# Performance work log

Hardware: AMD Instinct MI355X
Metric: run time of the kernel (lower is better)

## Reference

```python
import jax, jax.numpy as jnp
import numpy as np

EPS = 1e-5
K = 20


def knn(x, k):
    # x: (b, c, n) -> idx (b, n, k) of nearest neighbors (negative sq. distance, top-k)
    xx = jnp.sum(x * x, axis=1)                      # (b, n)
    inner = jnp.einsum('bcn,bcm->bnm', x, x)         # (b, n, n)
    neg_dist = -xx[:, :, None] + 2.0 * inner - xx[:, None, :]
    _, idx = jax.lax.top_k(neg_dist, k)
    return idx


def graph_feature(x, k):
    # x: (b, c, n) -> (b, 2c, n, k) with [neighbor - center, center]
    b, c, n = x.shape
    idx = knn(x, k)                                   # (b, n, k)
    xt = jnp.transpose(x, (0, 2, 1))                  # (b, n, c)
    nbr = jax.vmap(lambda xb, ib: xb[ib])(xt, idx)    # (b, n, k, c)
    ctr = xt[:, :, None, :]                           # (b, n, 1, c)
    f = jnp.concatenate([nbr - ctr, jnp.broadcast_to(ctr, (b, n, k, c))], axis=-1)
    return jnp.transpose(f, (0, 3, 1, 2))             # (b, 2c, n, k)


def conv_bn_lrelu2d(f, W, gamma, beta):
    # 1x1 Conv2d (no bias) + BatchNorm2d (batch stats) + LeakyReLU(0.2)
    y = jnp.einsum('oc,bcnk->bonk', W, f)
    m = jnp.mean(y, axis=(0, 2, 3), keepdims=True)
    v = jnp.var(y, axis=(0, 2, 3), keepdims=True)
    y = (y - m) * jax.lax.rsqrt(v + EPS) * gamma[None, :, None, None] + beta[None, :, None, None]
    return jnp.where(y >= 0, y, 0.2 * y)


def conv_bn_lrelu1d(f, W, gamma, beta):
    y = jnp.einsum('oc,bcn->bon', W, f)
    m = jnp.mean(y, axis=(0, 2), keepdims=True)
    v = jnp.var(y, axis=(0, 2), keepdims=True)
    y = (y - m) * jax.lax.rsqrt(v + EPS) * gamma[None, :, None] + beta[None, :, None]
    return jnp.where(y >= 0, y, 0.2 * y)


def setup_inputs() -> dict:
    key = jax.random.key(0)
    ks = jax.random.split(key, 16)
    B, N = 8, 1024
    x = jax.random.normal(ks[0], (B, 3, N), dtype=jnp.float32)
    def w(k_, o, c):
        return jax.random.normal(k_, (o, c), dtype=jnp.float32) * (1.0 / np.sqrt(c))
    W1 = w(ks[1], 64, 6)
    W2 = w(ks[2], 64, 128)
    W3 = w(ks[3], 128, 128)
    W4 = w(ks[4], 256, 256)
    W5 = w(ks[5], 1024, 512)
    def gb(k_, c):
        k1, k2 = jax.random.split(k_)
        return (1.0 + 0.1 * jax.random.normal(k1, (c,), dtype=jnp.float32),
                0.1 * jax.random.normal(k2, (c,), dtype=jnp.float32))
    g1, b1 = gb(ks[6], 64)
    g2, b2 = gb(ks[7], 64)
    g3, b3 = gb(ks[8], 128)
    g4, b4 = gb(ks[9], 256)
    g5, b5 = gb(ks[10], 1024)
    return dict(x=x, W1=W1, g1=g1, b1=b1, W2=W2, g2=g2, b2=b2,
                W3=W3, g3=g3, b3=b3, W4=W4, g4=g4, b4=b4,
                W5=W5, g5=g5, b5=b5)


def reference(x, W1, g1, b1, W2, g2, b2, W3, g3, b3, W4, g4, b4, W5, g5, b5):
    f = graph_feature(x, K)                           # (b, 6, n, k)
    x1 = jnp.max(conv_bn_lrelu2d(f, W1, g1, b1), axis=-1)   # (b, 64, n)
    f = graph_feature(x1, K)
    x2 = jnp.max(conv_bn_lrelu2d(f, W2, g2, b2), axis=-1)   # (b, 64, n)
    f = graph_feature(x2, K)
    x3 = jnp.max(conv_bn_lrelu2d(f, W3, g3, b3), axis=-1)   # (b, 128, n)
    f = graph_feature(x3, K)
    x4 = jnp.max(conv_bn_lrelu2d(f, W4, g4, b4), axis=-1)   # (b, 256, n)
    cat = jnp.concatenate([x1, x2, x3, x4], axis=1)          # (b, 512, n)
    y = conv_bn_lrelu1d(cat, W5, g5, b5)                     # (b, 1024, n)
    return jnp.max(y, axis=-1)                               # (b, 1024) global feature
```

## Files before the change

### kernel.cpp

```cpp
#include <hip/hip_runtime.h>
#include <math.h>

#define KK 20
#define NPTS 1024
#define BB 8
#define EPSF 1e-5f

__device__ __forceinline__ void select20f(float (&d)[16], int lane, int* orow)
{
  int keep = 0;
  for (int s = 0; s < KK; ++s) {
    float bd = d[0]; int bj = 0;
    #pragma unroll
    for (int j = 1; j < 16; ++j)
      if (d[j] > bd) { bd = d[j]; bj = j; }
    int bi = bj * 64 + lane;
    #pragma unroll
    for (int o = 1; o < 64; o <<= 1) {
      float od = __shfl_xor(bd, o, 64);
      int   oi = __shfl_xor(bi, o, 64);
      if (od > bd || (od == bd && oi < bi)) { bd = od; bi = oi; }
    }
    if (lane == s) keep = bi;
    if ((bi & 63) == lane) {
      int jw = bi >> 6;
      #pragma unroll
      for (int j = 0; j < 16; ++j)
        if (j == jw) d[j] = -INFINITY;
    }
  }
  if (lane < KK) orow[lane] = keep;
}

template <int C, int CEFF>
__global__ __launch_bounds__(512, 8) void knn8_kernel(
    const float* __restrict__ x, long bstride,
    int* __restrict__ idx_out)
{
  const int t = threadIdx.x, w = t >> 6, lane = t & 63;
  const int b = blockIdx.y;
  const int n0 = blockIdx.x * 8;
  const int p = n0 + w;
  __shared__ float xs2[2][NPTS * 2];
  __shared__ float xxs[NPTS];
  const float* xb = x + (long)b * bstride;

  float2 r2[4];
  #pragma unroll
  for (int j = 0; j < 4; ++j) {
    if (j < CEFF) r2[j] = *(const float2*)&xb[(long)j * NPTS + 2 * t];
    else          r2[j] = make_float2(0.f, 0.f);
  }

  float xx0 = 0.f, xx1 = 0.f;
  float dot[16];
  #pragma unroll
  for (int j = 0; j < 16; ++j) dot[j] = 0.f;

  for (int c0 = 0; c0 < C; c0 += 4) {
    __syncthreads();
    {
      float4 w0 = make_float4(r2[0].x, r2[1].x, r2[0].y, r2[1].y);
      float4 w1 = make_float4(r2[2].x, r2[3].x, r2[2].y, r2[3].y);
      *(float4*)&xs2[0][4 * t] = w0;
      *(float4*)&xs2[1][4 * t] = w1;
    }
    #pragma unroll
    for (int j = 0; j < 4; ++j) {
      xx0 = fmaf(r2[j].x, r2[j].x, xx0);
      xx1 = fmaf(r2[j].y, r2[j].y, xx1);
    }
    __syncthreads();
    if (c0 + 4 < C) {
      #pragma unroll
      for (int j = 0; j < 4; ++j)
        r2[j] = *(const float2*)&xb[(long)(c0 + 4 + j) * NPTS + 2 * t];
    }
    #pragma unroll
    for (int pr = 0; pr < 2; ++pr) {
      float2 cab = *(const float2*)&xs2[pr][p * 2];
      #pragma unroll
      for (int j = 0; j < 16; ++j) {
        float2 v = *(const float2*)&xs2[pr][(j * 64 + lane) * 2];
        dot[j] = fmaf(cab.x, v.x, dot[j]);
        dot[j] = fmaf(cab.y, v.y, dot[j]);
      }
    }
  }
  *(float2*)&xxs[2 * t] = make_float2(xx0, xx1);
  __syncthreads();

  const float xxP = xxs[p];
  #pragma unroll
  for (int j = 0; j < 16; ++j) {
    float xm = xxs[j * 64 + lane];
    dot[j] = (2.0f * dot[j] - xxP) - xm;
  }
  select20f(dot, lane, idx_out + ((long)b * NPTS + p) * KK);
}

template <typename AccT, int C, int O, int CB2, int TN>
__global__ __launch_bounds__(256) void cg_kernel(
    const float* __restrict__ x, long bstride,
    const float* __restrict__ W,
    AccT* __restrict__ Yc,
    AccT* __restrict__ G, long gbs)
{
  const int t = threadIdx.x, b = blockIdx.y;
  const int o = t & (O - 1);
  const int nbase = (t / O) * 16;
  const int nn0 = blockIdx.x * TN;
  __shared__ float s_wd[CB2 * O];
  __shared__ float s_w1[CB2 * O];
  __shared__ float s_xs[CB2 * TN];
  const float* xb = x + (long)b * bstride;

  AccT accC[16], accG[16];
  #pragma unroll
  for (int j = 0; j < 16; ++j) { accC[j] = (AccT)0; accG[j] = (AccT)0; }

  for (int c0 = 0; c0 < C; c0 += CB2) {
    __syncthreads();
    for (int i = t; i < CB2 * O; i += 256) {
      int oo = i / CB2, cc = i - oo * CB2;
      float a  = W[(long)oo * (2 * C) + c0 + cc];
      float b2 = W[(long)oo * (2 * C) + C + c0 + cc];
      s_wd[cc * O + oo] = b2 - a;
      s_w1[cc * O + oo] = a;
    }
    for (int i = t; i < CB2 * TN; i += 256) {
      int cc = i / TN, nn = i - cc * TN;
      s_xs[cc * TN + nn] = xb[(long)(c0 + cc) * NPTS + nn0 + nn];
    }
    __syncthreads();
    #pragma unroll
    for (int cc = 0; cc < CB2; ++cc) {
      float wd  = s_wd[cc * O + o];
      float w1v = s_w1[cc * O + o];
      #pragma unroll
      for (int j = 0; j < 16; ++j) {
        AccT xv = (AccT)s_xs[cc * TN + nbase + j];
        accC[j] += (AccT)wd  * xv;
        accG[j] += (AccT)w1v * xv;
      }
    }
  }
  #pragma unroll
  for (int j = 0; j < 16; ++j) {
    int n = nn0 + nbase + j;
    Yc[((long)b * NPTS + n) * O + o] = accC[j];
    G[(long)b * gbs + (long)n * O + o] = accG[j];
  }
}

template <typename AccT, int O, int NPT, int ITERS>
__global__ __launch_bounds__(256) void ec_max_kernel(
    const int* __restrict__ idx,
    const AccT* __restrict__ G, long gbs,
    const AccT* __restrict__ Yc,
    double* __restrict__ sums,
    AccT* __restrict__ yraw)
{
  const int t = threadIdx.x, b = blockIdx.y;
  const int o = t & (O - 1);
  const int np = t / O;
  const int LP = NPT * ITERS;
  const int n0 = blockIdx.x * LP;

  __shared__ int s_jj[8 * KK];
  __shared__ double reds[256];
  __shared__ double redq[256];

  for (int i = t; i < LP * KK; i += 256) {
    int l = i / KK, kk = i - l * KK;
    s_jj[i] = idx[((long)b * NPTS + n0 + l) * KK + kk];
  }
  __syncthreads();

  const AccT* Gb = G + (long)b * gbs + o;
  double accS = 0.0, accQ = 0.0;
  #pragma unroll
  for (int it = 0; it < ITERS; ++it) {
    const int l = it * NPT + np;
    const int n = n0 + l;
    AccT y0 = Yc[((long)b * NPTS + n) * O + o];
    AccT ps = (AccT)0, pq = (AccT)0, pm = (AccT)(-INFINITY);
    #pragma unroll
    for (int k = 0; k < KK; ++k) {
      int j = s_jj[l * KK + k];
      AccT v = Gb[(long)j * O] + y0;
      ps += v; pq += v * v;
      pm = (v > pm) ? v : pm;
    }
    yraw[((long)b * NPTS + n) * O + o] = pm;
    accS += (double)ps; accQ += (double)pq;
  }
  __syncthreads();
  reds[t] = accS; redq[t] = accQ;
  __syncthreads();
  if (t < O) {
    double s = 0.0, q = 0.0;
    #pragma unroll
    for (int g = 0; g < NPT; ++g) { s += reds[g * O + t]; q += redq[g * O + t]; }
    atomicAdd(&sums[t], s);
    atomicAdd(&sums[1024 + t], q);
  }
}

template <typename AccT, int O, int OL>
__global__ __launch_bounds__(256) void ec_norm(
    const AccT* __restrict__ yraw, const double* __restrict__ sums,
    const float* __restrict__ gamma, const float* __restrict__ beta,
    float* __restrict__ xout)
{
  int i = blockIdx.x * 256 + threadIdx.x;
  int n = i & (NPTS - 1);
  int o = (i >> 10) & (O - 1);
  int b = i >> (10 + OL);
  const double cnt = (double)BB * NPTS * KK;
  double m = sums[o] / cnt;
  double var = sums[1024 + o] / cnt - m * m;
  double inv = 1.0 / sqrt(var + (double)EPSF);
  AccT y = yraw[((long)b * NPTS + n) * O + o];
  AccT v = (y - (AccT)m) * (AccT)inv * (AccT)gamma[o] + (AccT)beta[o];
  v = (v >= (AccT)0) ? v : (AccT)0.2 * v;
  xout[(long)b * (512L * NPTS) + (long)o * NPTS + n] = (float)v;
}

__device__ inline unsigned fkey(float f) {
  unsigned u = __float_as_uint(f);
  return (u & 0x80000000u) ? ~u : (u | 0x80000000u);
}
__device__ inline float keyf(unsigned k) {
  return __uint_as_float((k & 0x80000000u) ? (k ^ 0x80000000u) : ~k);
}

#define WST2 260

__global__ __launch_bounds__(256, 4) void fin_fused(
    const float* __restrict__ cat, const float* __restrict__ W5,
    double* __restrict__ sums, unsigned* __restrict__ mkeys)
{
  const int nt = blockIdx.x, ot = blockIdx.y, t = threadIdx.x;
  const int w = t >> 6, lane = t & 63;
  const int col0 = nt * 32;
  const int b = col0 >> 10;
  const int nb = col0 & 1023;

  __shared__ float sm[16 * WST2 + 16 * 32];
  float* s_w = sm;
  float* s_f = sm + 16 * WST2;

  const int wrow0 = t >> 2, wcq = (t & 3) * 4;
  const float* wbase = W5 + ((long)(ot * 256 + wrow0)) * 512 + wcq;
  const int fcc = (2 * t) >> 5, fnn = (2 * t) & 31;
  const float* fbase = cat + ((long)b * 512 + fcc) * 1024 + nb + fnn;

  float4 rw[4];
  float2 rf;
  #pragma unroll
  for (int q = 0; q < 4; ++q)
    rw[q] = *(const float4*)&wbase[(long)(64 * q) * 512];
  rf = *(const float2*)fbase;

  float acc[4][8];
  #pragma unroll
  for (int r = 0; r < 4; ++r)
    #pragma unroll
    for (int j = 0; j < 8; ++j) acc[r][j] = 0.f;

  for (int c0 = 0; c0 < 512; c0 += 16) {
    __syncthreads();
    #pragma unroll
    for (int q = 0; q < 4; ++q) {
      float e[4] = {rw[q].x, rw[q].y, rw[q].z, rw[q].w};
      #pragma unroll
      for (int j = 0; j < 4; ++j)
        s_w[(wcq + j) * WST2 + wrow0 + 64 * q] = e[j];
    }
    *(float2*)&s_f[fcc * 32 + fnn] = rf;
    __syncthreads();
    if (c0 + 16 < 512) {
      #pragma unroll
      for (int q = 0; q < 4; ++q)
        rw[q] = *(const float4*)&wbase[(long)(64 * q) * 512 + c0 + 16];
      rf = *(const float2*)&fbase[(long)(c0 + 16) * 1024];
    }
    #pragma unroll
    for (int cc = 0; cc < 16; ++cc) {
      float4 wA = *(const float4*)&s_w[cc * WST2 + lane * 4];
      float4 f0 = *(const float4*)&s_f[cc * 32 + w * 8];
      float4 f1 = *(const float4*)&s_f[cc * 32 + w * 8 + 4];
      float wa[4] = {wA.x, wA.y, wA.z, wA.w};
      float fv[8] = {f0.x, f0.y, f0.z, f0.w, f1.x, f1.y, f1.z, f1.w};
      #pragma unroll
      for (int r = 0; r < 4; ++r)
        #pragma unroll
        for (int j = 0; j < 8; ++j)
          acc[r][j] += wa[r] * fv[j];
    }
  }

  float psum[4], psq[4], pmx[4];
  #pragma unroll
  for (int r = 0; r < 4; ++r) {
    psum[r] = 0.f; psq[r] = 0.f; pmx[r] = -INFINITY;
    #pragma unroll
    for (int j = 0; j < 8; ++j) {
      float v = acc[r][j];
      psum[r] += v; psq[r] += v * v; pmx[r] = fmaxf(pmx[r], v);
    }
  }
  __syncthreads();
  float* red_s = sm;
  float* red_q = sm + 1024;
  float* red_m = sm + 2048;
  #pragma unroll
  for (int r = 0; r < 4; ++r) {
    int oo = lane * 4 + r;
    red_s[w * 256 + oo] = psum[r];
    red_q[w * 256 + oo] = psq[r];
    red_m[w * 256 + oo] = pmx[r];
  }
  __syncthreads();
  {
    int oo = t;
    float s = 0.f, q = 0.f, m = -INFINITY;
    #pragma unroll
    for (int ww = 0; ww < 4; ++ww) {
      s += red_s[ww * 256 + oo];
      q += red_q[ww * 256 + oo];
      m = fmaxf(m, red_m[ww * 256 + oo]);
    }
    int o = ot * 256 + oo;
    atomicAdd(&sums[o], (double)s);
    atomicAdd(&sums[1024 + o], (double)q);
    atomicMax(&mkeys[b * 1024 + o], fkey(m));
  }
}

__global__ __launch_bounds__(256) void fin_norm(
    const unsigned* __restrict__ mkeys, const double* __restrict__ sums,
    const float* __restrict__ g, const float* __restrict__ bt,
    float* __restrict__ out)
{
  int i = blockIdx.x * 256 + threadIdx.x;
  int o = i & 1023;
  double m = sums[o] / 8192.0;
  double var = sums[1024 + o] / 8192.0 - m * m;
  float inv = (float)(1.0 / sqrt(var + (double)EPSF));
  float y = keyf(mkeys[i]);
  float v = (y - (float)m) * inv * g[o] + bt[o];
  out[i] = (v >= 0.f) ? v : 0.2f * v;
}

extern "C" void kernel_launch(void* const* d_in, const int* in_sizes, int n_in,
                              void* d_out, int out_size, void* d_ws, size_t ws_size,
                              hipStream_t stream)
{
  (void)in_sizes; (void)n_in; (void)out_size; (void)ws_size;
  const float* x0 = (const float*)d_in[0];
  const float* W1 = (const float*)d_in[1];
  const float* g1 = (const float*)d_in[2];
  const float* b1 = (const float*)d_in[3];
  const float* W2 = (const float*)d_in[4];
  const float* g2 = (const float*)d_in[5];
  const float* b2 = (const float*)d_in[6];
  const float* W3 = (const float*)d_in[7];
  const float* g3 = (const float*)d_in[8];
  const float* b3 = (const float*)d_in[9];
  const float* W4 = (const float*)d_in[10];
  const float* g4 = (const float*)d_in[11];
  const float* b4 = (const float*)d_in[12];
  const float* W5 = (const float*)d_in[13];
  const float* g5 = (const float*)d_in[14];
  const float* b5 = (const float*)d_in[15];
  float* outp = (float*)d_out;

  char* w = (char*)d_ws;
  double*   sums   = (double*)w;   w += 5 * 2048 * sizeof(double);
  unsigned* mkeys  = (unsigned*)w; w += (size_t)BB * 1024 * sizeof(unsigned);
  int*      idxbuf = (int*)w;      w += (size_t)BB * NPTS * KK * sizeof(int);
  char*     yraw   = w;            w += (size_t)BB * NPTS * 128 * sizeof(double);
  char*     ycbuf  = w;            w += (size_t)BB * NPTS * 128 * sizeof(double);
  float*    cat    = (float*)w;

  double* sumsL[5] = {sums, sums + 2048, sums + 4096, sums + 6144, sums + 8192};

  const long catbs = 512L * NPTS;
  float* gbase = cat + 256 * NPTS;

  dim3 gknn(NPTS / 8, BB);

  hipMemsetAsync(sums, 0, 5 * 2048 * sizeof(double) + (size_t)BB * 1024 * sizeof(unsigned),
                 stream);

  knn8_kernel<4, 3><<<gknn, 512, 0, stream>>>(x0, 3L * NPTS, idxbuf);
  cg_kernel<double, 3, 64, 3, 64><<<dim3(NPTS / 64, BB), 256, 0, stream>>>(
      x0, 3L * NPTS, W1, (double*)ycbuf, (double*)gbase, catbs / 2);
  ec_max_kernel<double, 64, 4, 2><<<dim3(NPTS / 8, BB), 256, 0, stream>>>(
      idxbuf, (const double*)gbase, catbs / 2, (const double*)ycbuf,
      sumsL[0], (double*)yraw);
  ec_norm<double, 64, 6><<<BB * 64 * NPTS / 256, 256, 0, stream>>>(
      (const double*)yraw, sumsL[0], g1, b1, cat);

  knn8_kernel<64, 64><<<gknn, 512, 0, stream>>>(cat, catbs, idxbuf);
  cg_kernel<double, 64, 64, 16, 64><<<dim3(NPTS / 64, BB), 256, 0, stream>>>(
      cat, catbs, W2, (double*)ycbuf, (double*)gbase, catbs / 2);
  ec_max_kernel<double, 64, 4, 2><<<dim3(NPTS / 8, BB), 256, 0, stream>>>(
      idxbuf, (const double*)gbase, catbs / 2, (const double*)ycbuf,
      sumsL[1], (double*)yraw);
  ec_norm<double, 64, 6><<<BB * 64 * NPTS / 256, 256, 0, stream>>>(
      (const double*)yraw, sumsL[1], g2, b2, cat + 64 * NPTS);

  knn8_kernel<64, 64><<<gknn, 512, 0, stream>>>(cat + 64 * NPTS, catbs, idxbuf);
  cg_kernel<double, 64, 128, 16, 32><<<dim3(NPTS / 32, BB), 256, 0, stream>>>(
      cat + 64 * NPTS, catbs, W3, (double*)ycbuf, (double*)gbase, catbs / 2);
  ec_max_kernel<double, 128, 2, 4><<<dim3(NPTS / 8, BB), 256, 0, stream>>>(
      idxbuf, (const double*)gbase, catbs / 2, (const double*)ycbuf,
      sumsL[2], (double*)yraw);
  ec_norm<double, 128, 7><<<BB * 128 * NPTS / 256, 256, 0, stream>>>(
      (const double*)yraw, sumsL[2], g3, b3, cat + 128 * NPTS);

  knn8_kernel<128, 128><<<gknn, 512, 0, stream>>>(cat + 128 * NPTS, catbs, idxbuf);
  cg_kernel<float, 128, 256, 16, 16><<<dim3(NPTS / 16, BB), 256, 0, stream>>>(
      cat + 128 * NPTS, catbs, W4, (float*)ycbuf, gbase, catbs);
  ec_max_kernel<float, 256, 1, 4><<<dim3(NPTS / 4, BB), 256, 0, stream>>>(
      idxbuf, (const float*)gbase, catbs, (const float*)ycbuf,
      sumsL[3], (float*)yraw);
  ec_norm<float, 256, 8><<<BB * 256 * NPTS / 256, 256, 0, stream>>>(
      (const float*)yraw, sumsL[3], g4, b4, cat + 256 * NPTS);

  dim3 gf(256, 4);
  fin_fused<<<gf, 256, 0, stream>>>(cat, W5, sumsL[4], mkeys);
  fin_norm<<<BB * 1024 / 256, 256, 0, stream>>>(mkeys, sumsL[4], g5, b5, outp);
}
```

Measured before the change: 779.5 us.

## Compute two query points per wave in kNN and use DPP reductions

The kNN kernel now has each wave handle two query points, so every shared-memory candidate load is reused for two dot products, and the grid is halved to match. The top-20 selection replaces the linear 16-way argmax with a tree reduction and does the first four cross-lane steps with DPP moves instead of shuffles. The cost is more registers per thread (launch bounds lowered to 4 blocks) and two selection passes done one after another per wave, which reduces occupancy and latency hiding.

New measurement: 969.7 us. 1.24x slower.

```diff
diff --git a/kernel.cpp b/kernel.cpp
--- a/kernel.cpp
+++ b/kernel.cpp
@@ -6,21 +6,54 @@
 #define BB 8
 #define EPSF 1e-5f
 
+__device__ __forceinline__ void kmerge(float& bd, int& bi, float od, int oi) {
+  if (od > bd || (od == bd && oi < bi)) { bd = od; bi = oi; }
+}
+
+template <int CTRL>
+__device__ __forceinline__ void dpp_step(float& bd, int& bi) {
+  int vd = __builtin_amdgcn_update_dpp(0, __float_as_int(bd), CTRL, 0xF, 0xF, true);
+  int vi = __builtin_amdgcn_update_dpp(0, bi, CTRL, 0xF, 0xF, true);
+  kmerge(bd, bi, __int_as_float(vd), vi);
+}
+
 __device__ __forceinline__ void select20f(float (&d)[16], int lane, int* orow)
 {
   int keep = 0;
   for (int s = 0; s < KK; ++s) {
-    float bd = d[0]; int bj = 0;
-    #pragma unroll
-    for (int j = 1; j < 16; ++j)
-      if (d[j] > bd) { bd = d[j]; bj = j; }
-    int bi = bj * 64 + lane;
-    #pragma unroll
-    for (int o = 1; o < 64; o <<= 1) {
-      float od = __shfl_xor(bd, o, 64);
-      int   oi = __shfl_xor(bi, o, 64);
-      if (od > bd || (od == bd && oi < bi)) { bd = od; bi = oi; }
-    }
+    float tv[8]; int tj[8];
+    #pragma unroll
+    for (int j = 0; j < 8; ++j) {
+      bool bt = d[2 * j + 1] > d[2 * j];
+      tv[j] = bt ? d[2 * j + 1] : d[2 * j];
+      tj[j] = bt ? 2 * j + 1 : 2 * j;
+    }
+    #pragma unroll
+    for (int j = 0; j < 4; ++j) {
+      bool bt = tv[2 * j + 1] > tv[2 * j];
+      tv[j] = bt ? tv[2 * j + 1] : tv[2 * j];
+      tj[j] = bt ? tj[2 * j + 1] : tj[2 * j];
+    }
+    #pragma unroll
+    for (int j = 0; j < 2; ++j) {
+      bool bt = tv[2 * j + 1] > tv[2 * j];
+      tv[j] = bt ? tv[2 * j + 1] : tv[2 * j];
+      tj[j] = bt ? tj[2 * j + 1] : tj[2 * j];
+    }
+    bool bt = tv[1] > tv[0];
+    float bd = bt ? tv[1] : tv[0];
+    int   bj = bt ? tj[1] : tj[0];
+    int   bi = bj * 64 + lane;
+
+    dpp_step<0xB1>(bd, bi);
+    dpp_step<0x4E>(bd, bi);
+    dpp_step<0x124>(bd, bi);
+    dpp_step<0x128>(bd, bi);
+    { float od = __shfl_xor(bd, 16, 64); int oi = __shfl_xor(bi, 16, 64);
+      kmerge(bd, bi, od, oi); }
+    { float od = __shfl_xor(bd, 32, 64); int oi = __shfl_xor(bi, 32, 64);
+      kmerge(bd, bi, od, oi); }
+
     if (lane == s) keep = bi;
     if ((bi & 63) == lane) {
       int jw = bi >> 6;
@@ -33,14 +66,14 @@
 }
 
 template <int C, int CEFF>
-__global__ __launch_bounds__(512, 8) void knn8_kernel(
+__global__ __launch_bounds__(512, 4) void knn9_kernel(
     const float* __restrict__ x, long bstride,
     int* __restrict__ idx_out)
 {
   const int t = threadIdx.x, w = t >> 6, lane = t & 63;
   const int b = blockIdx.y;
-  const int n0 = blockIdx.x * 8;
-  const int p = n0 + w;
+  const int n0 = blockIdx.x * 16;
+  const int pa = n0 + 2 * w, pb = pa + 1;
   __shared__ float xs2[2][NPTS * 2];
   __shared__ float xxs[NPTS];
   const float* xb = x + (long)b * bstride;
@@ -53,9 +86,9 @@
   }
 
   float xx0 = 0.f, xx1 = 0.f;
-  float dot[16];
-  #pragma unroll
-  for (int j = 0; j < 16; ++j) dot[j] = 0.f;
+  float dotA[16], dotB[16];
+  #pragma unroll
+  for (int j = 0; j < 16; ++j) { dotA[j] = 0.f; dotB[j] = 0.f; }
 
   for (int c0 = 0; c0 < C; c0 += 4) {
     __syncthreads();
@@ -78,25 +111,30 @@
     }
     #pragma unroll
     for (int pr = 0; pr < 2; ++pr) {
-      float2 cab = *(const float2*)&xs2[pr][p * 2];
+      float2 cA = *(const float2*)&xs2[pr][pa * 2];
+      float2 cB = *(const float2*)&xs2[pr][pb * 2];
       #pragma unroll
       for (int j = 0; j < 16; ++j) {
         float2 v = *(const float2*)&xs2[pr][(j * 64 + lane) * 2];
-        dot[j] = fmaf(cab.x, v.x, dot[j]);
-        dot[j] = fmaf(cab.y, v.y, dot[j]);
+        dotA[j] = fmaf(cA.x, v.x, dotA[j]);
+        dotA[j] = fmaf(cA.y, v.y, dotA[j]);
+        dotB[j] = fmaf(cB.x, v.x, dotB[j]);
+        dotB[j] = fmaf(cB.y, v.y, dotB[j]);
       }
     }
   }
   *(float2*)&xxs[2 * t] = make_float2(xx0, xx1);
   __syncthreads();
 
-  const float xxP = xxs[p];
+  const float xxA = xxs[pa], xxB = xxs[pb];
   #pragma unroll
   for (int j = 0; j < 16; ++j) {
     float xm = xxs[j * 64 + lane];
-    dot[j] = (2.0f * dot[j] - xxP) - xm;
-  }
-  select20f(dot, lane, idx_out + ((long)b * NPTS + p) * KK);
+    dotA[j] = (2.0f * dotA[j] - xxA) - xm;
+    dotB[j] = (2.0f * dotB[j] - xxB) - xm;
+  }
+  select20f(dotA, lane, idx_out + ((long)b * NPTS + pa) * KK);
+  select20f(dotB, lane, idx_out + ((long)b * NPTS + pb) * KK);
 }
 
 template <typename AccT, int C, int O, int CB2, int TN>
@@ -390,12 +428,12 @@
   const long catbs = 512L * NPTS;
   float* gbase = cat + 256 * NPTS;
 
-  dim3 gknn(NPTS / 8, BB);
+  dim3 gknn(NPTS / 16, BB);
 
   hipMemsetAsync(sums, 0, 5 * 2048 * sizeof(double) + (size_t)BB * 1024 * sizeof(unsigned),
                  stream);
 
-  knn8_kernel<4, 3><<<gknn, 512, 0, stream>>>(x0, 3L * NPTS, idxbuf);
+  knn9_kernel<4, 3><<<gknn, 512, 0, stream>>>(x0, 3L * NPTS, idxbuf);
   cg_kernel<double, 3, 64, 3, 64><<<dim3(NPTS / 64, BB), 256, 0, stream>>>(
       x0, 3L * NPTS, W1, (double*)ycbuf, (double*)gbase, catbs / 2);
   ec_max_kernel<double, 64, 4, 2><<<dim3(NPTS / 8, BB), 256, 0, stream>>>(
@@ -404,7 +442,7 @@
   ec_norm<double, 64, 6><<<BB * 64 * NPTS / 256, 256, 0, stream>>>(
       (const double*)yraw, sumsL[0], g1, b1, cat);
 
-  knn8_kernel<64, 64><<<gknn, 512, 0, stream>>>(cat, catbs, idxbuf);
+  knn9_kernel<64, 64><<<gknn, 512, 0, stream>>>(cat, catbs, idxbuf);
   cg_kernel<double, 64, 64, 16, 64><<<dim3(NPTS / 64, BB), 256, 0, stream>>>(
       cat, catbs, W2, (double*)ycbuf, (double*)gbase, catbs / 2);
   ec_max_kernel<double, 64, 4, 2><<<dim3(NPTS / 8, BB), 256, 0, stream>>>(
@@ -413,7 +451,7 @@
   ec_norm<double, 64, 6><<<BB * 64 * NPTS / 256, 256, 0, stream>>>(
       (const double*)yraw, sumsL[1], g2, b2, cat + 64 * NPTS);
 
-  knn8_kernel<64, 64><<<gknn, 512, 0, stream>>>(cat + 64 * NPTS, catbs, idxbuf);
+  knn9_kernel<64, 64><<<gknn, 512, 0, stream>>>(cat + 64 * NPTS, catbs, idxbuf);
   cg_kernel<double, 64, 128, 16, 32><<<dim3(NPTS / 32, BB), 256, 0, stream>>>(
       cat + 64 * NPTS, catbs, W3, (double*)ycbuf, (double*)gbase, catbs / 2);
   ec_max_kernel<double, 128, 2, 4><<<dim3(NPTS / 8, BB), 256, 0, stream>>>(
@@ -422,7 +460,7 @@
   ec_norm<double, 128, 7><<<BB * 128 * NPTS / 256, 256, 0, stream>>>(
       (const double*)yraw, sumsL[2], g3, b3, cat + 128 * NPTS);
 
-  knn8_kernel<128, 128><<<gknn, 512, 0, stream>>>(cat + 128 * NPTS, catbs, idxbuf);
+  knn9_kernel<128, 128><<<gknn, 512, 0, stream>>>(cat + 128 * NPTS, catbs, idxbuf);
   cg_kernel<float, 128, 256, 16, 16><<<dim3(NPTS / 16, BB), 256, 0, stream>>>(
       cat + 128 * NPTS, catbs, W4, (float*)ycbuf, gbase, catbs);
   ec_max_kernel<float, 256, 1, 4><<<dim3(NPTS / 4, BB), 256, 0, stream>>>(
```
